# Kernel optimization log

Hardware: AMD Instinct MI355X
Metric: run time of the kernel (lower is better)

The kernel has to match this reference:

```python
import jax, jax.numpy as jnp
import numpy as np

N_NODES = 100000
N_EDGES = 3200000
IN_FEATS = 256
N_HIDDEN = 256
N_CLASSES = 40


def setup_inputs() -> dict:
    key = jax.random.key(0)
    ks = jax.random.split(key, 8)
    features = jax.random.normal(ks[0], (N_NODES, IN_FEATS), dtype=jnp.float32)
    src = jax.random.randint(ks[1], (N_EDGES,), 0, N_NODES, dtype=jnp.int64)
    dst = jax.random.randint(ks[2], (N_EDGES,), 0, N_NODES, dtype=jnp.int64)
    # Glorot-ish init scaled down for stability
    W0 = jax.random.normal(ks[3], (IN_FEATS, N_HIDDEN), dtype=jnp.float32) * (1.0 / np.sqrt(IN_FEATS))
    W1 = jax.random.normal(ks[4], (N_HIDDEN, N_HIDDEN), dtype=jnp.float32) * (1.0 / np.sqrt(N_HIDDEN))
    W2 = jax.random.normal(ks[5], (N_HIDDEN, N_CLASSES), dtype=jnp.float32) * (1.0 / np.sqrt(N_HIDDEN))
    b0 = jnp.zeros((N_HIDDEN,), jnp.float32)
    b1 = jnp.zeros((N_HIDDEN,), jnp.float32)
    b2 = jnp.zeros((N_CLASSES,), jnp.float32)
    return {"features": features, "src": src, "dst": dst,
            "W0": W0, "b0": b0, "W1": W1, "b1": b1, "W2": W2, "b2": b2}


def _degree_norms(src, dst, n_nodes):
    ones = jnp.ones(src.shape[0], jnp.float32)
    deg_out = jax.ops.segment_sum(ones, src, num_segments=n_nodes)
    deg_in = jax.ops.segment_sum(ones, dst, num_segments=n_nodes)
    # DGL norm='both': clamp degree to >=1 before rsqrt
    norm_out = jax.lax.rsqrt(jnp.maximum(deg_out, 1.0))  # applied on source side
    norm_in = jax.lax.rsqrt(jnp.maximum(deg_in, 1.0))    # applied on dest side
    return norm_out, norm_in


def _graph_conv(h, src, dst, norm_out, norm_in, W, b, activation):
    # h: [N, Fin]. norm='both': D_in^{-1/2} * A * (D_out^{-1/2} * h) @ W + b
    in_f, out_f = W.shape
    h = h * norm_out[:, None]
    if in_f > out_f:
        # mult weight first to reduce message width (DGL optimization, same math)
        h = h @ W
        agg = jax.ops.segment_sum(h[src], dst, num_segments=h.shape[0])
    else:
        agg = jax.ops.segment_sum(h[src], dst, num_segments=h.shape[0])
        agg = agg @ W
    out = agg * norm_in[:, None] + b
    if activation is not None:
        out = activation(out)
    return out


def reference(features, src, dst, W0, b0, W1, b1, W2, b2):
    n = features.shape[0]
    norm_out, norm_in = _degree_norms(src, dst, n)
    h = _graph_conv(features, src, dst, norm_out, norm_in, W0, b0, jax.nn.relu)
    h = _graph_conv(h, src, dst, norm_out, norm_in, W1, b1, jax.nn.relu)
    h = _graph_conv(h, src, dst, norm_out, norm_in, W2, b2, None)
    return h
```

## Files before the change

kernel.cpp:

```cpp
#include <hip/hip_runtime.h>

#define NN 100000
#define NE 3200000
#define F 256
#define NCLS 40
#define NC 391
#define NBLK_H 256
#define EPB (NE / NBLK_H)
#define CW 25000

using h4 = __attribute__((ext_vector_type(4))) _Float16;
using h8 = __attribute__((ext_vector_type(8))) _Float16;
using f4 = __attribute__((ext_vector_type(4))) float;

__global__ __launch_bounds__(512) void hist_k(const int* __restrict__ src,
                                              const int* __restrict__ dst,
                                              unsigned* __restrict__ pcnt,
                                              unsigned* __restrict__ pcc) {
    __shared__ unsigned hsrc[CW];
    __shared__ unsigned hc[NC];
    int t = threadIdx.x, b = blockIdx.x;
    for (int i = t; i < CW; i += 512) hsrc[i] = 0;
    for (int i = t; i < NC; i += 512) hc[i] = 0;
    __syncthreads();
    int beg = b * EPB, end = beg + EPB;
    for (int e = beg + t; e < end; e += 512) {
        int s = src[e];
        atomicAdd(&hsrc[s >> 2], 1u << (8 * (s & 3)));
        atomicAdd(&hc[dst[e] >> 8], 1u);
    }
    __syncthreads();
    unsigned* pc = pcnt + (size_t)b * CW;
    for (int i = t; i < CW; i += 512) pc[i] = hsrc[i];
    unsigned* pb = pcc + (size_t)b * NC;
    for (int i = t; i < NC; i += 512) pb[i] = hc[i];
}

__global__ __launch_bounds__(256) void redA_k(const unsigned* __restrict__ pcnt,
                                              unsigned* __restrict__ pl,
                                              unsigned* __restrict__ ph) {
    int w = blockIdx.x * 256 + threadIdx.x;
    if (w >= CW) return;
    int g = blockIdx.y;
    unsigned lo = 0, hi = 0;
    for (int b = g * 32; b < g * 32 + 32; b++) {
        unsigned v = pcnt[(size_t)b * CW + w];
        lo += (v & 255u) | (((v >> 8) & 255u) << 16);
        hi += ((v >> 16) & 255u) | ((v >> 24) << 16);
    }
    pl[(size_t)g * CW + w] = lo;
    ph[(size_t)g * CW + w] = hi;
}

__global__ void nout2_k(const unsigned* __restrict__ pl, const unsigned* __restrict__ ph,
                        float* __restrict__ nout) {
    int w = blockIdx.x * blockDim.x + threadIdx.x;
    if (w >= CW) return;
    unsigned lo = 0, hi = 0;
#pragma unroll
    for (int g = 0; g < 8; g++) { lo += pl[(size_t)g * CW + w]; hi += ph[(size_t)g * CW + w]; }
    float4 o;
    o.x = rsqrtf(fmaxf((float)(lo & 0xFFFFu), 1.f));
    o.y = rsqrtf(fmaxf((float)(lo >> 16), 1.f));
    o.z = rsqrtf(fmaxf((float)(hi & 0xFFFFu), 1.f));
    o.w = rsqrtf(fmaxf((float)(hi >> 16), 1.f));
    *(float4*)(nout + w * 4) = o;
}

__global__ __launch_bounds__(256) void offsets_k(const unsigned* __restrict__ pcc,
                                                 unsigned* __restrict__ curoff,
                                                 unsigned* __restrict__ totals) {
    __shared__ unsigned sh[256];
    int c = blockIdx.x, t = threadIdx.x;
    unsigned v = pcc[(size_t)t * NC + c];
    sh[t] = v;
    __syncthreads();
    for (int off = 1; off < 256; off <<= 1) {
        unsigned x = (t >= off) ? sh[t - off] : 0;
        __syncthreads();
        sh[t] += x;
        __syncthreads();
    }
    curoff[(size_t)t * NC + c] = sh[t] - v;
    if (t == 255) totals[c] = sh[255];
}

__global__ __launch_bounds__(512) void base_k(const unsigned* __restrict__ totals,
                                              int* __restrict__ cbase) {
    __shared__ unsigned sh[512];
    int t = threadIdx.x;
    unsigned v = (t < NC) ? totals[t] : 0;
    sh[t] = v;
    __syncthreads();
    for (int off = 1; off < 512; off <<= 1) {
        unsigned x = (t >= off) ? sh[t - off] : 0;
        __syncthreads();
        sh[t] += x;
        __syncthreads();
    }
    if (t < NC) cbase[t] = (int)(sh[t] - v);
    if (t == 0) cbase[NC] = NE;
}

__global__ __launch_bounds__(512) void p1scat_k(const int* __restrict__ src,
                                                const int* __restrict__ dst,
                                                const int* __restrict__ cbase,
                                                const unsigned* __restrict__ curoff,
                                                unsigned* __restrict__ ebuf) {
    __shared__ int cur[NC];
    int t = threadIdx.x, b = blockIdx.x;
    for (int i = t; i < NC; i += 512)
        cur[i] = cbase[i] + (int)curoff[(size_t)b * NC + i];
    __syncthreads();
    int beg = b * EPB, end = beg + EPB;
    for (int e = beg + t; e < end; e += 512) {
        int d = dst[e];
        int p = atomicAdd(&cur[d >> 8], 1);
        ebuf[p] = (unsigned)src[e] | ((unsigned)(d & 255) << 17);
    }
}

__global__ __launch_bounds__(512) void p2build_k(const int* __restrict__ cbase,
                                                 const unsigned* __restrict__ ebuf,
                                                 int* __restrict__ csr_src,
                                                 int* __restrict__ row_ptr,
                                                 float* __restrict__ nin) {
    __shared__ int cnt[256], cur[256], sh[256];
    int c = blockIdx.x, t = threadIdx.x;
    int beg = cbase[c], end = cbase[c + 1];
    if (t < 256) cnt[t] = 0;
    __syncthreads();
    for (int e = beg + t; e < end; e += 512)
        atomicAdd(&cnt[(ebuf[e] >> 17) & 255], 1);
    __syncthreads();
    int v = 0;
    if (t < 256) { v = cnt[t]; sh[t] = v; }
    __syncthreads();
    for (int off = 1; off < 256; off <<= 1) {
        int x = (t < 256 && t >= off) ? sh[t - off] : 0;
        __syncthreads();
        if (t < 256) sh[t] += x;
        __syncthreads();
    }
    if (t < 256) {
        int pref = sh[t] - v;
        int node = c * 256 + t;
        if (node <= NN) row_ptr[node] = beg + pref;
        if (node < NN)  nin[node] = rsqrtf(fmaxf((float)v, 1.f));
        cur[t] = pref;
    }
    if (c == 0 && t == 0) row_ptr[NN] = NE;
    __syncthreads();
    for (int e = beg + t; e < end; e += 512) {
        unsigned w = ebuf[e];
        int p = atomicAdd(&cur[(w >> 17) & 255], 1);
        csr_src[beg + p] = (int)(w & 0x1FFFFu);
    }
}

__global__ void conv_fused_k(const float4* __restrict__ fin, const float* __restrict__ nout,
                             h4* __restrict__ fout,
                             const float* __restrict__ W0, const float* __restrict__ W1,
                             const float* __restrict__ W2,
                             _Float16* __restrict__ Wt0, _Float16* __restrict__ Wt1,
                             _Float16* __restrict__ Wt2) {
    int i = blockIdx.x * blockDim.x + threadIdx.x;
    const int N4 = NN * 64;
    if (i < N4) {
        float s = nout[i >> 6];
        float4 v = fin[i];
        h4 o;
        o[0] = (_Float16)(v.x * s);
        o[1] = (_Float16)(v.y * s);
        o[2] = (_Float16)(v.z * s);
        o[3] = (_Float16)(v.w * s);
        fout[i] = o;
    } else {
        int j = i - N4;
        if (j < 65536) {
            int n = j >> 8, k = (j & 255) ^ ((n & 7) << 3);
            Wt0[j] = (_Float16)W0[k * 256 + n];
        } else if (j < 131072) {
            int jj = j - 65536;
            int n = jj >> 8, k = (jj & 255) ^ ((n & 7) << 3);
            Wt1[jj] = (_Float16)W1[k * 256 + n];
        } else if (j < 147456) {
            int jj = j - 131072;
            int n = jj >> 8, k = (jj & 255) ^ ((n & 7) << 3);
            Wt2[jj] = (n < NCLS) ? (_Float16)W2[k * NCLS + n] : (_Float16)0.0f;
        }
    }
}

__global__ __launch_bounds__(256) void agg256h_k(
        const int* __restrict__ row_ptr, const int* __restrict__ csr_src,
        const _Float16* __restrict__ h, _Float16* __restrict__ agg, int nN) {
    int node = (blockIdx.x * blockDim.x + threadIdx.x) >> 6;
    int lane = threadIdx.x & 63;
    if (node >= nN) return;
    int half = lane >> 5, col = lane & 31;
    int beg = row_ptr[node], end = row_ptr[node + 1];
    f4 a[4][2];
#pragma unroll
    for (int u = 0; u < 4; u++) { a[u][0] = (f4){0,0,0,0}; a[u][1] = (f4){0,0,0,0}; }
    int e = beg;
    for (; e + 7 < end; e += 8) {
        int s[4];
#pragma unroll
        for (int u = 0; u < 4; u++) s[u] = csr_src[e + 2 * u + half];
        h8 v[4];
#pragma unroll
        for (int u = 0; u < 4; u++)
            v[u] = *(const h8*)(h + (size_t)s[u] * F + col * 8);
#pragma unroll
        for (int u = 0; u < 4; u++)
#pragma unroll
            for (int j = 0; j < 8; j++) a[u][j >> 2][j & 3] += (float)v[u][j];
    }
    for (int t = e + half; t < end; t += 2) {
        h8 v = *(const h8*)(h + (size_t)csr_src[t] * F + col * 8);
#pragma unroll
        for (int j = 0; j < 8; j++) a[0][j >> 2][j & 3] += (float)v[j];
    }
    float r[8];
#pragma unroll
    for (int j = 0; j < 8; j++)
        r[j] = (a[0][j >> 2][j & 3] + a[1][j >> 2][j & 3])
             + (a[2][j >> 2][j & 3] + a[3][j >> 2][j & 3]);
#pragma unroll
    for (int j = 0; j < 8; j++) r[j] += __shfl_xor(r[j], 32);
    if (half == 0) {
        h8 o;
#pragma unroll
        for (int j = 0; j < 8; j++) o[j] = (_Float16)r[j];
        *(h8*)(agg + (size_t)node * F + col * 8) = o;
    }
}

__global__ __launch_bounds__(256) void agg64h_k(
        const int* __restrict__ row_ptr, const int* __restrict__ csr_src,
        const _Float16* __restrict__ t3, const float* __restrict__ nin,
        const float* __restrict__ b2, float* __restrict__ out, int nN) {
    int node = (blockIdx.x * blockDim.x + threadIdx.x) >> 6;
    int lane = threadIdx.x & 63;
    if (node >= nN) return;
    int grp = lane >> 3, c = lane & 7;
    int beg = row_ptr[node], end = row_ptr[node + 1];
    float a0[8], a1[8];
#pragma unroll
    for (int j = 0; j < 8; j++) { a0[j] = 0.f; a1[j] = 0.f; }
    int e = beg;
    for (; e + 15 < end; e += 16) {
        int s0 = csr_src[e + grp], s1 = csr_src[e + 8 + grp];
        h8 v0 = *(const h8*)(t3 + (size_t)s0 * 64 + c * 8);
        h8 v1 = *(const h8*)(t3 + (size_t)s1 * 64 + c * 8);
#pragma unroll
        for (int j = 0; j < 8; j++) { a0[j] += (float)v0[j]; a1[j] += (float)v1[j]; }
    }
    for (int t = e + grp; t < end; t += 8) {
        h8 v = *(const h8*)(t3 + (size_t)csr_src[t] * 64 + c * 8);
#pragma unroll
        for (int j = 0; j < 8; j++) a0[j] += (float)v[j];
    }
    float r[8];
#pragma unroll
    for (int j = 0; j < 8; j++) {
        r[j] = a0[j] + a1[j];
        r[j] += __shfl_xor(r[j], 8);
        r[j] += __shfl_xor(r[j], 16);
        r[j] += __shfl_xor(r[j], 32);
    }
    if (grp == 0 && c < 5) {
        float ni = nin[node];
        float4 o;
        o.x = r[0] * ni + b2[c * 8 + 0];
        o.y = r[1] * ni + b2[c * 8 + 1];
        o.z = r[2] * ni + b2[c * 8 + 2];
        o.w = r[3] * ni + b2[c * 8 + 3];
        *(float4*)(out + (size_t)node * NCLS + c * 8) = o;
        o.x = r[4] * ni + b2[c * 8 + 4];
        o.y = r[5] * ni + b2[c * 8 + 5];
        o.z = r[6] * ni + b2[c * 8 + 6];
        o.w = r[7] * ni + b2[c * 8 + 7];
        *(float4*)(out + (size_t)node * NCLS + c * 8 + 4) = o;
    }
}

__global__ __launch_bounds__(1024) void gemm0_k(
        const _Float16* __restrict__ A, const _Float16* __restrict__ Wt,
        _Float16* __restrict__ C, int M,
        const float* __restrict__ nin, const float* __restrict__ nout,
        const float* __restrict__ bias) {
    __shared__ _Float16 lds[256 * 256];
    char* ldsb = (char*)lds;
    const int tid  = threadIdx.x;
    const int lane = tid & 63;
    const int w    = tid >> 6;
    const int row0 = blockIdx.x * 256;

#pragma unroll
    for (int i = 0; i < 8; i++) {
        int idx = (i * 1024 + tid) * 8;
        *(h8*)(ldsb + idx * 2) = *(const h8*)(Wt + idx);
    }

    int arow = row0 + w * 16 + (lane & 15);
    if (arow >= M) arow = M - 1;
    const _Float16* Ap = A + (size_t)arow * 256 + (lane >> 4) * 8;
    h8 areg[8];
#pragma unroll
    for (int i = 0; i < 8; i++) areg[i] = *(const h8*)(Ap + i * 32);

    __syncthreads();

    f4 acc[16];
#pragma unroll
    for (int n = 0; n < 16; n++) acc[n] = (f4){0.f, 0.f, 0.f, 0.f};

#pragma unroll
    for (int k0 = 0; k0 < 8; k0++) {
        int kb = (k0 * 32 + (lane >> 4) * 8) * 2;
#pragma unroll
        for (int n = 0; n < 16; n++) {
            int r    = n * 16 + (lane & 15);
            int byte = r * 512 + kb;
            h8 bf = *(const h8*)(ldsb + (byte ^ ((r & 7) << 4)));
            acc[n] = __builtin_amdgcn_mfma_f32_16x16x32_f16(areg[k0], bf, acc[n], 0, 0, 0);
        }
    }

    __syncthreads();

    const int g  = lane >> 4;
    const int rb = row0 + w * 16 + g * 4;
    float si[4], so[4];
#pragma unroll
    for (int r = 0; r < 4; r++) {
        int rr = rb + r; if (rr >= M) rr = M - 1;
        si[r] = nin[rr];
        so[r] = nout[rr];
    }
    char* warea = ldsb + w * 8192;
#pragma unroll
    for (int n = 0; n < 16; n++) {
        float bb = bias[n * 16 + (lane & 15)];
#pragma unroll
        for (int r = 0; r < 4; r++) {
            float x = fmaxf(acc[n][r] * si[r] + bb, 0.f) * so[r];
            int lrow = g * 4 + r;
            int lcol = n * 16 + (lane & 15);
            *(_Float16*)(warea + (size_t)(lrow * 256 + lcol) * 2) = (_Float16)x;
        }
    }

    _Float16* Crow = C + (size_t)(row0 + w * 16) * 256;
#pragma unroll
    for (int i = 0; i < 8; i++) {
        int off  = i * 1024 + lane * 16;
        int lrow = off >> 9;
        int grow = row0 + w * 16 + lrow;
        h8 v = *(const h8*)(warea + off);
        if (grow < M) *(h8*)((char*)Crow + off) = v;
    }
}

__global__ __launch_bounds__(1024) void gemm12_k(
        const _Float16* __restrict__ A, const _Float16* __restrict__ Wt1s,
        const _Float16* __restrict__ Wt2s, _Float16* __restrict__ t3, int M,
        const float* __restrict__ nin, const float* __restrict__ nout,
        const float* __restrict__ bias) {
    __shared__ _Float16 lds[256 * 256];
    char* ldsb = (char*)lds;
    const int tid  = threadIdx.x;
    const int lane = tid & 63;
    const int w    = tid >> 6;
    const int row0 = blockIdx.x * 256;

#pragma unroll
    for (int i = 0; i < 8; i++) {
        int idx = (i * 1024 + tid) * 8;
        *(h8*)(ldsb + idx * 2) = *(const h8*)(Wt1s + idx);
    }

    int arow = row0 + w * 16 + (lane & 15);
    if (arow >= M) arow = M - 1;
    const _Float16* Ap = A + (size_t)arow * 256 + (lane >> 4) * 8;
    h8 areg[8];
#pragma unroll
    for (int i = 0; i < 8; i++) areg[i] = *(const h8*)(Ap + i * 32);

    __syncthreads();

    f4 acc[16];
#pragma unroll
    for (int n = 0; n < 16; n++) acc[n] = (f4){0.f, 0.f, 0.f, 0.f};
#pragma unroll
    for (int k0 = 0; k0 < 8; k0++) {
        int kb = (k0 * 32 + (lane >> 4) * 8) * 2;
#pragma unroll
        for (int n = 0; n < 16; n++) {
            int r    = n * 16 + (lane & 15);
            int byte = r * 512 + kb;
            h8 bf = *(const h8*)(ldsb + (byte ^ ((r & 7) << 4)));
            acc[n] = __builtin_amdgcn_mfma_f32_16x16x32_f16(areg[k0], bf, acc[n], 0, 0, 0);
        }
    }

    __syncthreads();

    const int g  = lane >> 4;
    const int rb = row0 + w * 16 + g * 4;
    float si[4], so[4];
#pragma unroll
    for (int r = 0; r < 4; r++) {
        int rr = rb + r; if (rr >= M) rr = M - 1;
        si[r] = nin[rr];
        so[r] = nout[rr];
    }
    char* warea = ldsb + w * 8192;
#pragma unroll
    for (int n = 0; n < 16; n++) {
        float bb = bias[n * 16 + (lane & 15)];
#pragma unroll
        for (int r = 0; r < 4; r++) {
            float x = fmaxf(acc[n][r] * si[r] + bb, 0.f) * so[r];
            int lrow = g * 4 + r;
            int lcol = n * 16 + (lane & 15);
            int byte = lrow * 512 + lcol * 2;
            *(_Float16*)(warea + (byte ^ ((lrow & 7) << 4))) = (_Float16)x;
        }
    }

    h8 areg2[8];
    {
        int lr = lane & 15;
#pragma unroll
        for (int k0 = 0; k0 < 8; k0++) {
            int byte = lr * 512 + k0 * 64 + (lane >> 4) * 16;
            areg2[k0] = *(const h8*)(warea + (byte ^ ((lr & 7) << 4)));
        }
    }
    __syncthreads();

#pragma unroll
    for (int i = 0; i < 2; i++) {
        int idx = (i * 1024 + tid) * 8;
        *(h8*)(ldsb + idx * 2) = *(const h8*)(Wt2s + idx);
    }
    __syncthreads();

    f4 acc2[4];
#pragma unroll
    for (int n = 0; n < 4; n++) acc2[n] = (f4){0.f, 0.f, 0.f, 0.f};
#pragma unroll
    for (int k0 = 0; k0 < 8; k0++) {
        int kb = k0 * 64 + (lane >> 4) * 16;
#pragma unroll
        for (int n = 0; n < 4; n++) {
            int r    = n * 16 + (lane & 15);
            int byte = r * 512 + kb;
            h8 bf = *(const h8*)(ldsb + (byte ^ ((r & 7) << 4)));
            acc2[n] = __builtin_amdgcn_mfma_f32_16x16x32_f16(areg2[k0], bf, acc2[n], 0, 0, 0);
        }
    }

    char* tarea = ldsb + 32768 + w * 2048;
#pragma unroll
    for (int n = 0; n < 4; n++)
#pragma unroll
        for (int r = 0; r < 4; r++) {
            int lrow = g * 4 + r;
            int c = n * 16 + (lane & 15);
            *(_Float16*)(tarea + lrow * 128 + c * 2) = (_Float16)acc2[n][r];
        }
#pragma unroll
    for (int i = 0; i < 2; i++) {
        int off  = i * 1024 + lane * 16;
        int lrow = off >> 7;
        int grow = row0 + w * 16 + lrow;
        h8 v = *(const h8*)(tarea + off);
        if (grow < M) *(h8*)((char*)t3 + (size_t)grow * 128 + (off & 127)) = v;
    }
}

extern "C" void kernel_launch(void* const* d_in, const int* in_sizes, int n_in,
                              void* d_out, int out_size, void* d_ws, size_t ws_size,
                              hipStream_t stream) {
    const float* features = (const float*)d_in[0];
    const int*   src      = (const int*)d_in[1];
    const int*   dst      = (const int*)d_in[2];
    const float* W0       = (const float*)d_in[3];
    const float* b0       = (const float*)d_in[4];
    const float* W1       = (const float*)d_in[5];
    const float* b1       = (const float*)d_in[6];
    const float* W2       = (const float*)d_in[7];
    const float* b2       = (const float*)d_in[8];
    float* out = (float*)d_out;

    char* ws = (char*)d_ws;
    const size_t H_BYTES = (size_t)NN * F * 2;
    _Float16* hA   = (_Float16*)(ws);
    _Float16* hB   = (_Float16*)(ws + H_BYTES);
    _Float16* t3h  = (_Float16*)(ws + 2 * H_BYTES);
    char* q = ws + 2 * H_BYTES + (size_t)NN * 64 * 2;
    int* csr_src    = (int*)q;               q += (size_t)NE * 4;
    unsigned* ebuf  = (unsigned*)q;          q += (size_t)NE * 4;
    unsigned* pcnt  = (unsigned*)q;          q += (size_t)NBLK_H * CW * 4;
    unsigned* pl    = (unsigned*)q;          q += (size_t)8 * CW * 4;
    unsigned* ph    = (unsigned*)q;          q += (size_t)8 * CW * 4;
    unsigned* pcc   = (unsigned*)q;          q += (size_t)NBLK_H * NC * 4 + 1024;
    unsigned* curoff= (unsigned*)q;          q += (size_t)NBLK_H * NC * 4 + 1024;
    char* p = q;
    const size_t SB = 401408;
    unsigned* totals = (unsigned*)(p + 0 * SB);
    int*   cbase   = (int*)(p + 1 * SB);
    int*   row_ptr = (int*)(p + 2 * SB);
    float* nout    = (float*)(p + 3 * SB);
    float* nin     = (float*)(p + 4 * SB);
    _Float16* Wt0  = (_Float16*)(p + 5 * SB);
    _Float16* Wt1  = (_Float16*)(p + 5 * SB + 131072);
    _Float16* Wt2  = (_Float16*)(p + 5 * SB + 262144);

    const int AGG_BLOCKS = (NN * 64 + 255) / 256;
    const int GB = (NN + 255) / 256;

    hist_k<<<NBLK_H, 512, 0, stream>>>(src, dst, pcnt, pcc);
    {
        dim3 rg((CW + 255) / 256, 8);
        redA_k<<<rg, 256, 0, stream>>>(pcnt, pl, ph);
    }
    nout2_k<<<(CW + 255) / 256, 256, 0, stream>>>(pl, ph, nout);
    offsets_k<<<NC, 256, 0, stream>>>(pcc, curoff, totals);
    base_k<<<1, 512, 0, stream>>>(totals, cbase);
    p1scat_k<<<NBLK_H, 512, 0, stream>>>(src, dst, cbase, curoff, ebuf);
    p2build_k<<<NC, 512, 0, stream>>>(cbase, ebuf, csr_src, row_ptr, nin);

    {
        int total = NN * 64 + 147456;
        conv_fused_k<<<(total + 255) / 256, 256, 0, stream>>>(
            (const float4*)features, nout, (h4*)hB, W0, W1, W2, Wt0, Wt1, Wt2);
    }

    agg256h_k<<<AGG_BLOCKS, 256, 0, stream>>>(row_ptr, csr_src, hB, hA, NN);
    gemm0_k<<<GB, 1024, 0, stream>>>(hA, Wt0, hB, NN, nin, nout, b0);

    agg256h_k<<<AGG_BLOCKS, 256, 0, stream>>>(row_ptr, csr_src, hB, hA, NN);
    gemm12_k<<<GB, 1024, 0, stream>>>(hA, Wt1, Wt2, t3h, NN, nin, nout, b1);

    agg64h_k<<<AGG_BLOCKS, 256, 0, stream>>>(row_ptr, csr_src, t3h, nin, b2, out, NN);
}
```

Baseline: 837.0 us.

## Sort CSR neighbors by source range and sweep aggregation in lockstep windows

The CSR build now sorts each destination's neighbor list by source-id window (4096-node buckets) using an 8192-bin local counting sort instead of a per-destination bucket. A new first-layer aggregation kernel has each wave handle 8 destination nodes and sweep the 25 source windows in lockstep. Gathers from all waves then touch a narrow slice of the feature table at the same time, which should improve L2 locality. This costs more control flow, repeated index reloads, lower per-wave memory parallelism and extra LDS in the build kernel.

```diff
diff --git a/kernel.cpp b/kernel.cpp
--- a/kernel.cpp
+++ b/kernel.cpp
@@ -125,36 +125,52 @@
                                                  int* __restrict__ csr_src,
                                                  int* __restrict__ row_ptr,
                                                  float* __restrict__ nin) {
-    __shared__ int cnt[256], cur[256], sh[256];
+    __shared__ int cnt[8192];
+    __shared__ int sh[512];
     int c = blockIdx.x, t = threadIdx.x;
     int beg = cbase[c], end = cbase[c + 1];
-    if (t < 256) cnt[t] = 0;
-    __syncthreads();
-    for (int e = beg + t; e < end; e += 512)
-        atomicAdd(&cnt[(ebuf[e] >> 17) & 255], 1);
-    __syncthreads();
-    int v = 0;
-    if (t < 256) { v = cnt[t]; sh[t] = v; }
-    __syncthreads();
-    for (int off = 1; off < 256; off <<= 1) {
-        int x = (t < 256 && t >= off) ? sh[t - off] : 0;
-        __syncthreads();
-        if (t < 256) sh[t] += x;
-        __syncthreads();
-    }
-    if (t < 256) {
-        int pref = sh[t] - v;
-        int node = c * 256 + t;
-        if (node <= NN) row_ptr[node] = beg + pref;
-        if (node < NN)  nin[node] = rsqrtf(fmaxf((float)v, 1.f));
-        cur[t] = pref;
-    }
-    if (c == 0 && t == 0) row_ptr[NN] = NE;
+    for (int i = t; i < 8192; i += 512) cnt[i] = 0;
     __syncthreads();
     for (int e = beg + t; e < end; e += 512) {
         unsigned w = ebuf[e];
-        int p = atomicAdd(&cur[(w >> 17) & 255], 1);
-        csr_src[beg + p] = (int)(w & 0x1FFFFu);
+        int key = (int)(((w >> 17) & 255u) << 5) | (int)((w & 0x1FFFFu) >> 12);
+        atomicAdd(&cnt[key], 1);
+    }
+    __syncthreads();
+    int loc[16];
+    int base16 = t * 16;
+    int lsum = 0;
+#pragma unroll
+    for (int i = 0; i < 16; i++) { loc[i] = cnt[base16 + i]; lsum += loc[i]; }
+    sh[t] = lsum;
+    __syncthreads();
+    for (int off = 1; off < 512; off <<= 1) {
+        int x = (t >= off) ? sh[t - off] : 0;
+        __syncthreads();
+        sh[t] += x;
+        __syncthreads();
+    }
+    int run = sh[t] - lsum;
+#pragma unroll
+    for (int i = 0; i < 16; i++) { cnt[base16 + i] = run; run += loc[i]; }
+    __syncthreads();
+    if (t < 256) {
+        int node = c * 256 + t;
+        int start = cnt[t << 5];
+        int next  = (t == 255) ? (end - beg) : cnt[(t + 1) << 5];
+        if (node < NN) {
+            row_ptr[node] = beg + start;
+            nin[node] = rsqrtf(fmaxf((float)(next - start), 1.f));
+        }
+    }
+    if (c == 0 && t == 0) row_ptr[NN] = NE;
+    __syncthreads();
+    for (int e = beg + t; e < end; e += 512) {
+        unsigned w = ebuf[e];
+        int s = (int)(w & 0x1FFFFu);
+        int key = (int)(((w >> 17) & 255u) << 5) | (s >> 12);
+        int p = atomicAdd(&cnt[key], 1);
+        csr_src[beg + p] = s;
     }
 }
 
@@ -192,6 +208,79 @@
     }
 }
 
+__global__ __launch_bounds__(256) void agg256sw_k(
+        const int* __restrict__ row_ptr, const int* __restrict__ csr_src,
+        const _Float16* __restrict__ h, _Float16* __restrict__ agg, int nN) {
+    int wid  = (blockIdx.x * blockDim.x + threadIdx.x) >> 6;
+    int lane = threadIdx.x & 63;
+    int half = lane >> 5, col = lane & 31;
+    int node0 = wid * 8;
+    if (node0 >= nN) return;
+
+    int c0, c1, c2, c3, e0, e1, e2, e3;
+    {
+        int nd;
+        nd = node0 + 0 + half; if (nd < nN) { c0 = row_ptr[nd]; e0 = row_ptr[nd + 1]; } else { c0 = e0 = 0; }
+        nd = node0 + 2 + half; if (nd < nN) { c1 = row_ptr[nd]; e1 = row_ptr[nd + 1]; } else { c1 = e1 = 0; }
+        nd = node0 + 4 + half; if (nd < nN) { c2 = row_ptr[nd]; e2 = row_ptr[nd + 1]; } else { c2 = e2 = 0; }
+        nd = node0 + 6 + half; if (nd < nN) { c3 = row_ptr[nd]; e3 = row_ptr[nd + 1]; } else { c3 = e3 = 0; }
+    }
+    f4 a0[2] = {(f4){0,0,0,0},(f4){0,0,0,0}}, a1[2] = {(f4){0,0,0,0},(f4){0,0,0,0}};
+    f4 a2[2] = {(f4){0,0,0,0},(f4){0,0,0,0}}, a3[2] = {(f4){0,0,0,0},(f4){0,0,0,0}};
+
+    for (int r = 0; r < 25; r++) {
+        while (true) {
+            bool g0 = false, g1 = false, g2 = false, g3 = false;
+            int s0 = 0, s1 = 0, s2 = 0, s3 = 0;
+            if (c0 < e0) { s0 = csr_src[c0]; g0 = ((s0 >> 12) == r); }
+            if (c1 < e1) { s1 = csr_src[c1]; g1 = ((s1 >> 12) == r); }
+            if (c2 < e2) { s2 = csr_src[c2]; g2 = ((s2 >> 12) == r); }
+            if (c3 < e3) { s3 = csr_src[c3]; g3 = ((s3 >> 12) == r); }
+            if (!(g0 | g1 | g2 | g3)) break;
+            h8 v0, v1, v2, v3;
+            if (g0) { v0 = *(const h8*)(h + (size_t)s0 * F + col * 8); c0++; }
+            if (g1) { v1 = *(const h8*)(h + (size_t)s1 * F + col * 8); c1++; }
+            if (g2) { v2 = *(const h8*)(h + (size_t)s2 * F + col * 8); c2++; }
+            if (g3) { v3 = *(const h8*)(h + (size_t)s3 * F + col * 8); c3++; }
+#pragma unroll
+            for (int j = 0; j < 8; j++) {
+                if (g0) a0[j >> 2][j & 3] += (float)v0[j];
+                if (g1) a1[j >> 2][j & 3] += (float)v1[j];
+                if (g2) a2[j >> 2][j & 3] += (float)v2[j];
+                if (g3) a3[j >> 2][j & 3] += (float)v3[j];
+            }
+        }
+    }
+    {
+        int nd;
+        h8 o;
+        nd = node0 + 0 + half;
+        if (nd < nN) {
+#pragma unroll
+            for (int j = 0; j < 8; j++) o[j] = (_Float16)a0[j >> 2][j & 3];
+            *(h8*)(agg + (size_t)nd * F + col * 8) = o;
+        }
+        nd = node0 + 2 + half;
+        if (nd < nN) {
+#pragma unroll
+            for (int j = 0; j < 8; j++) o[j] = (_Float16)a1[j >> 2][j & 3];
+            *(h8*)(agg + (size_t)nd * F + col * 8) = o;
+        }
+        nd = node0 + 4 + half;
+        if (nd < nN) {
+#pragma unroll
+            for (int j = 0; j < 8; j++) o[j] = (_Float16)a2[j >> 2][j & 3];
+            *(h8*)(agg + (size_t)nd * F + col * 8) = o;
+        }
+        nd = node0 + 6 + half;
+        if (nd < nN) {
+#pragma unroll
+            for (int j = 0; j < 8; j++) o[j] = (_Float16)a3[j >> 2][j & 3];
+            *(h8*)(agg + (size_t)nd * F + col * 8) = o;
+        }
+    }
+}
+
 __global__ __launch_bounds__(256) void agg256h_k(
         const int* __restrict__ row_ptr, const int* __restrict__ csr_src,
         const _Float16* __restrict__ h, _Float16* __restrict__ agg, int nN) {
@@ -522,6 +611,7 @@
     _Float16* Wt2  = (_Float16*)(p + 5 * SB + 262144);
 
     const int AGG_BLOCKS = (NN * 64 + 255) / 256;
+    const int SW_BLOCKS  = ((NN + 7) / 8 * 64 + 255) / 256;
     const int GB = (NN + 255) / 256;
 
     hist_k<<<NBLK_H, 512, 0, stream>>>(src, dst, pcnt, pcc);
@@ -541,7 +631,7 @@
             (const float4*)features, nout, (h4*)hB, W0, W1, W2, Wt0, Wt1, Wt2);
     }
 
-    agg256h_k<<<AGG_BLOCKS, 256, 0, stream>>>(row_ptr, csr_src, hB, hA, NN);
+    agg256sw_k<<<SW_BLOCKS, 256, 0, stream>>>(row_ptr, csr_src, hB, hA, NN);
     gemm0_k<<<GB, 1024, 0, stream>>>(hA, Wt0, hB, NN, nin, nout, b0);
 
     agg256h_k<<<AGG_BLOCKS, 256, 0, stream>>>(row_ptr, csr_src, hB, hA, NN);
```

After: 1.054 ms. 1.26x slower.
